# Optimization experiments

Measured on AMD Instinct MI355X. Metric: run time of the kernel, lower is better.

The kernel has to match this reference:

```python
import jax, jax.numpy as jnp
import numpy as np

U, I, D, B, E = 100000, 50000, 64, 4, 2000000

def setup_inputs() -> dict:
    key = jax.random.key(0)
    k1, k2, k3, k4, k5, k6, k7 = jax.random.split(key, 7)
    user_embedding = jax.random.normal(k1, (U, D), dtype=jnp.float32) * 0.1
    item_embedding = jax.random.normal(k2, (I, D), dtype=jnp.float32) * 0.1
    rows = jax.random.randint(k3, (B, E), 0, U, dtype=jnp.int32)
    cols = jax.random.randint(k4, (B, E), 0, I, dtype=jnp.int32)
    # normalized-adjacency-like small positive values
    vals = jax.random.uniform(k5, (B, E), dtype=jnp.float32) * 0.05
    u_w = jax.random.normal(k6, (D, D), dtype=jnp.float32) * (1.0 / np.sqrt(D))
    i_w = jax.random.normal(k7, (D, D), dtype=jnp.float32) * (1.0 / np.sqrt(D))
    return {"user_embedding": user_embedding, "item_embedding": item_embedding,
            "rows": rows, "cols": cols, "vals": vals, "u_w": u_w, "i_w": i_w}

def reference(user_embedding, item_embedding, rows, cols, vals, u_w, i_w):
    n_users = user_embedding.shape[0]
    n_items = item_embedding.shape[0]

    # per-behavior spmm: A @ item_emb -> [U, D]; AT @ user_emb -> [I, D]
    def spmm_user(r, c, v):
        return jax.ops.segment_sum(v[:, None] * item_embedding[c], r,
                                   num_segments=n_users)

    def spmm_item(r, c, v):
        return jax.ops.segment_sum(v[:, None] * user_embedding[r], c,
                                   num_segments=n_items)

    user_stack = jax.vmap(spmm_user)(rows, cols, vals)  # [B, U, D]
    item_stack = jax.vmap(spmm_item)(rows, cols, vals)  # [B, I, D]

    user_emb = jax.nn.sigmoid(jnp.mean(user_stack, axis=0) @ u_w)   # [U, D]
    item_emb = jax.nn.sigmoid(jnp.mean(item_stack, axis=0) @ i_w)   # [I, D]
    user_embs = jax.nn.sigmoid(jnp.einsum('bud,de->bue', user_stack, u_w))  # [B, U, D]
    item_embs = jax.nn.sigmoid(jnp.einsum('bid,de->bie', item_stack, i_w))  # [B, I, D]
    return user_emb, item_emb, user_embs, item_embs
```

## Files before the change

### kernel.cpp

```cpp
#include <hip/hip_runtime.h>

#define U_N 100000
#define I_N 50000
#define D_N 64
#define B_N 4
#define E_N 2000000

#define EDGES   (B_N * E_N)
#define NSC_U   (U_N / 8)
#define NSC_I   (I_N / 8)
#define CROW    12544
#define NBLK    256
#define EPB     (EDGES / NBLK)
#define CAP     1536
#define XSTR    36
#define SC_T    13


__global__ __launch_bounds__(256) void cvt_kernel(const float* __restrict__ ue,
                                                  const float* __restrict__ ie,
                                                  unsigned short* __restrict__ u16,
                                                  unsigned short* __restrict__ i16) {
    int i = blockIdx.x * 256 + threadIdx.x;
    int nu = U_N * D_N;
    int ni = I_N * D_N;
    if (i < nu) {
        unsigned u = __float_as_uint(ue[i]);
        u += 0x7FFFu + ((u >> 16) & 1u);
        u16[i] = (unsigned short)(u >> 16);
    } else if (i < nu + ni) {
        int j = i - nu;
        unsigned u = __float_as_uint(ie[j]);
        u += 0x7FFFu + ((u >> 16) & 1u);
        i16[j] = (unsigned short)(u >> 16);
    }
}

__global__ __launch_bounds__(512) void bhist_kernel(const int* __restrict__ keys,
                                                    int nsc,
                                                    int* __restrict__ cnt) {
    __shared__ int h[CROW];
    for (int i = threadIdx.x; i < nsc; i += 512) h[i] = 0;
    __syncthreads();
    int lb = ((blockIdx.x & 7) << 5) | (blockIdx.x >> 3);
    int base = lb * EPB;
    for (int i = threadIdx.x; i < EPB; i += 512)
        atomicAdd(&h[keys[base + i] >> 3], 1);
    __syncthreads();
    int* row = cnt + (size_t)lb * CROW;
    for (int i = threadIdx.x; i < nsc; i += 512) row[i] = h[i];
}

__global__ __launch_bounds__(512) void scan_tot(const int* __restrict__ cnt,
                                                int nsc, int* __restrict__ cnt_ch) {
    int c = blockIdx.x * 512 + threadIdx.x;
    if (c >= nsc) return;
    int s = 0;
    for (int lb = 0; lb < NBLK; ++lb) s += cnt[(size_t)lb * CROW + c];
    cnt_ch[c] = s;
}

__global__ __launch_bounds__(1024) void scan_ex(const int* __restrict__ cnt_ch,
                                                int nsc, int* __restrict__ off_ch) {
    int t = threadIdx.x;
    int loc[SC_T]; int s = 0;
#pragma unroll
    for (int j = 0; j < SC_T; ++j) {
        int idx = t * SC_T + j;
        int c = (idx < nsc) ? cnt_ch[idx] : 0;
        loc[j] = s; s += c;
    }
    __shared__ int sm[1024];
    int mine = s; sm[t] = s; __syncthreads();
    for (int o = 1; o < 1024; o <<= 1) {
        int a = (t >= o) ? sm[t - o] : 0;
        __syncthreads(); sm[t] += a; __syncthreads();
    }
    int pre = sm[t] - mine;
#pragma unroll
    for (int j = 0; j < SC_T; ++j) {
        int idx = t * SC_T + j;
        if (idx < nsc) off_ch[idx] = pre + loc[j];
    }
}

__global__ __launch_bounds__(512) void scan_cur(int* __restrict__ cnt,
                                                const int* __restrict__ off_ch,
                                                int nsc) {
    int c = blockIdx.x * 512 + threadIdx.x;
    if (c >= nsc) return;
    int run = off_ch[c];
    for (int lb = 0; lb < NBLK; ++lb) {
        int v = cnt[(size_t)lb * CROW + c];
        cnt[(size_t)lb * CROW + c] = run;
        run += v;
    }
}

__global__ __launch_bounds__(512) void cplace_kernel(const int* __restrict__ keys,
                                                     const int* __restrict__ srcs,
                                                     const float* __restrict__ vals,
                                                     const int* __restrict__ cur_g,
                                                     int nsc,
                                                     uint2* __restrict__ pay) {
    __shared__ int cur[CROW];
    int lb = ((blockIdx.x & 7) << 5) | (blockIdx.x >> 3);
    const int* row = cur_g + (size_t)lb * CROW;
    for (int i = threadIdx.x; i < nsc; i += 512) cur[i] = row[i];
    __syncthreads();
    int base = lb * EPB;
    int b = lb >> 6;
    for (int i = threadIdx.x; i < EPB; i += 512) {
        int gi = base + i;
        int k = keys[gi];
        float v = vals[gi];
        int src = srcs[gi];
        int pos = atomicAdd(&cur[k >> 3], 1);
        pay[pos] = make_uint2(((unsigned)(((k & 7) << 2) | b) << 17) | (unsigned)src,
                              __float_as_uint(v));
    }
}

__global__ __launch_bounds__(512) void fused_kernel(
        const unsigned short* __restrict__ emb16,
        const float* __restrict__ W,
        const int* __restrict__ off_ch,
        const int* __restrict__ cnt_ch,
        const uint2* __restrict__ pay,
        float* __restrict__ embs,
        float* __restrict__ mean_out,
        int nrows) {
    int g = blockIdx.x;
    int start = off_ch[g], n = cnt_ch[g];
    int t = threadIdx.x, w = t >> 6, lane = t & 63;

    __shared__ uint2 st[CAP];
    __shared__ uint2 st2[CAP];
    __shared__ int c32[32];
    __shared__ int bstart[33];
    float* xs = (float*)st;

    if (n <= CAP) {
        if (t < 32) c32[t] = 0;
        __syncthreads();
        for (int i = t; i < n; i += 512) {
            uint2 p = pay[start + i];
            st[i] = p;
            atomicAdd(&c32[p.x >> 17], 1);
        }
        __syncthreads();
        if (t == 0) {
            int s = 0;
            for (int b2 = 0; b2 < 32; ++b2) {
                bstart[b2] = s; s += c32[b2]; c32[b2] = bstart[b2];
            }
            bstart[32] = s;
        }
        __syncthreads();
        for (int i = t; i < n; i += 512) {
            uint2 p = st[i];
            int pos = atomicAdd(&c32[p.x >> 17], 1);
            st2[pos] = p;
        }
        __syncthreads();

        int qt = lane >> 4, ql = lane & 15;
        float4 a0, a1, a2, a3;
#define ACC_BIN(AQ, Q)                                                        \
        {                                                                     \
            int s0 = bstart[w * 4 + (Q)], s1 = bstart[w * 4 + (Q) + 1];       \
            AQ = make_float4(0.f, 0.f, 0.f, 0.f);                             \
            for (int j = s0; j < s1; j += 4) {                                \
                int idx = j + qt;                                             \
                int jj = idx < s1 ? idx : s1 - 1;                             \
                uint2 p = st2[jj];                                            \
                float v = (idx < s1) ? __uint_as_float(p.y) : 0.f;            \
                uint2 x = *((const uint2*)(emb16 +                            \
                              (size_t)(p.x & 0x1FFFFu) * 64) + ql);           \
                AQ.x = fmaf(v, __uint_as_float(x.x << 16), AQ.x);             \
                AQ.y = fmaf(v, __uint_as_float(x.x & 0xFFFF0000u), AQ.y);     \
                AQ.z = fmaf(v, __uint_as_float(x.y << 16), AQ.z);             \
                AQ.w = fmaf(v, __uint_as_float(x.y & 0xFFFF0000u), AQ.w);     \
            }                                                                 \
            AQ.x += __shfl_xor(AQ.x, 16); AQ.x += __shfl_xor(AQ.x, 32);       \
            AQ.y += __shfl_xor(AQ.y, 16); AQ.y += __shfl_xor(AQ.y, 32);       \
            AQ.z += __shfl_xor(AQ.z, 16); AQ.z += __shfl_xor(AQ.z, 32);       \
            AQ.w += __shfl_xor(AQ.w, 16); AQ.w += __shfl_xor(AQ.w, 32);       \
        }
        ACC_BIN(a0, 0)
        ACC_BIN(a1, 1)
        ACC_BIN(a2, 2)
        ACC_BIN(a3, 3)
#undef ACC_BIN
        if (qt == 0) {
            *(float4*)&xs[(4 * ql + 0) * XSTR + w * 4] =
                make_float4(a0.x, a1.x, a2.x, a3.x);
            *(float4*)&xs[(4 * ql + 1) * XSTR + w * 4] =
                make_float4(a0.y, a1.y, a2.y, a3.y);
            *(float4*)&xs[(4 * ql + 2) * XSTR + w * 4] =
                make_float4(a0.z, a1.z, a2.z, a3.z);
            *(float4*)&xs[(4 * ql + 3) * XSTR + w * 4] =
                make_float4(a0.w, a1.w, a2.w, a3.w);
        }
    } else {
        for (int i = t; i < 64 * XSTR; i += 512) xs[i] = 0.f;
        __syncthreads();
        for (int j = w; j < n; j += 8) {
            uint2 pv = pay[start + j];
            float x = __uint_as_float(
                (unsigned)emb16[(size_t)(pv.x & 0x1FFFFu) * 64 + lane] << 16);
            atomicAdd(&xs[lane * XSTR + (int)(pv.x >> 17)],
                      __uint_as_float(pv.y) * x);
        }
        __syncthreads();
    }

    float y[4] = {0.f, 0.f, 0.f, 0.f};
#pragma unroll 4
    for (int d = 0; d < 64; ++d) {
        float4 xq = *(const float4*)&xs[d * XSTR + w * 4];
        float wv = W[d * 64 + lane];
        y[0] = fmaf(xq.x, wv, y[0]);
        y[1] = fmaf(xq.y, wv, y[1]);
        y[2] = fmaf(xq.z, wv, y[2]);
        y[3] = fmaf(xq.w, wv, y[3]);
    }
    int row = g * 8 + w;
#pragma unroll
    for (int q = 0; q < 4; ++q)
        embs[((long long)q * nrows + row) * 64 + lane] =
            1.f / (1.f + __expf(-y[q]));
    float m = 0.25f * (y[0] + y[1] + y[2] + y[3]);
    mean_out[(long long)row * 64 + lane] = 1.f / (1.f + __expf(-m));
}

__global__ void scatter_atomic_kernel(const float* __restrict__ user_emb,
                                      const float* __restrict__ item_emb,
                                      const int* __restrict__ rows,
                                      const int* __restrict__ cols,
                                      const float* __restrict__ vals,
                                      float* __restrict__ stack_u,
                                      float* __restrict__ stack_i) {
    long long tid = (long long)blockIdx.x * blockDim.x + threadIdx.x;
    long long e  = tid >> 4;
    int lane = (int)(tid & 15);
    if (e >= (long long)EDGES) return;
    int b = (int)(e / E_N);
    int r = rows[e];
    int c = cols[e];
    float v = vals[e];
    const float4* irow = (const float4*)(item_emb + (long long)c * D_N);
    const float4* urow = (const float4*)(user_emb + (long long)r * D_N);
    float4 iv = irow[lane];
    float4 uv = urow[lane];
    float* du = stack_u + ((long long)b * U_N + r) * D_N + lane * 4;
    float* di = stack_i + ((long long)b * I_N + c) * D_N + lane * 4;
    atomicAdd(du + 0, v * iv.x);
    atomicAdd(du + 1, v * iv.y);
    atomicAdd(du + 2, v * iv.z);
    atomicAdd(du + 3, v * iv.w);
    atomicAdd(di + 0, v * uv.x);
    atomicAdd(di + 1, v * uv.y);
    atomicAdd(di + 2, v * uv.z);
    atomicAdd(di + 3, v * uv.w);
}

template <int NROWS>
__global__ __launch_bounds__(64) void transform_kernel(
        float* __restrict__ stack,
        const float* __restrict__ W,
        float* __restrict__ mean_out) {
    const int row = blockIdx.x;
    const int j   = threadIdx.x;
    __shared__ float xs[B_N][D_N];
#pragma unroll
    for (int b = 0; b < B_N; ++b)
        xs[b][j] = stack[((long long)b * NROWS + row) * D_N + j];
    __syncthreads();
    float acc[B_N] = {0.f, 0.f, 0.f, 0.f};
#pragma unroll 8
    for (int d = 0; d < D_N; ++d) {
        float w = W[d * D_N + j];
#pragma unroll
        for (int b = 0; b < B_N; ++b)
            acc[b] += xs[b][d] * w;
    }
    float m = 0.25f * (acc[0] + acc[1] + acc[2] + acc[3]);
#pragma unroll
    for (int b = 0; b < B_N; ++b)
        stack[((long long)b * NROWS + row) * D_N + j] =
            1.0f / (1.0f + __expf(-acc[b]));
    mean_out[(long long)row * D_N + j] = 1.0f / (1.0f + __expf(-m));
}

extern "C" void kernel_launch(void* const* d_in, const int* in_sizes, int n_in,
                              void* d_out, int out_size, void* d_ws, size_t ws_size,
                              hipStream_t stream) {
    const float* user_emb = (const float*)d_in[0];
    const float* item_emb = (const float*)d_in[1];
    const int*   rows     = (const int*)  d_in[2];
    const int*   cols     = (const int*)  d_in[3];
    const float* vals     = (const float*)d_in[4];
    const float* u_w      = (const float*)d_in[5];
    const float* i_w      = (const float*)d_in[6];

    float* out = (float*)d_out;
    float* user_mean = out;
    float* item_mean = out + (long long)U_N * D_N;
    float* stack_u   = item_mean + (long long)I_N * D_N;
    float* stack_i   = stack_u + (long long)B_N * U_N * D_N;

    int* cnt    = (int*)d_ws;
    int* cnt_ch = cnt + (size_t)NBLK * CROW;
    int* off_ch = cnt_ch + CROW;
    uint2* pay  = (uint2*)(off_ch + CROW);
    unsigned short* user16 = (unsigned short*)(pay + EDGES);
    unsigned short* item16 = user16 + (size_t)U_N * D_N;
    size_t needed = ((size_t)NBLK * CROW + 2 * CROW) * 4 +
                    (size_t)EDGES * 8 + (size_t)(U_N + I_N) * D_N * 2;

    if (ws_size >= needed) {
        int ncvt = (U_N + I_N) * D_N;
        cvt_kernel<<<(ncvt + 255) / 256, 256, 0, stream>>>(user_emb, item_emb,
                                                           user16, item16);
        bhist_kernel<<<NBLK, 512, 0, stream>>>(rows, NSC_U, cnt);
        scan_tot<<<(NSC_U + 511) / 512, 512, 0, stream>>>(cnt, NSC_U, cnt_ch);
        scan_ex<<<1, 1024, 0, stream>>>(cnt_ch, NSC_U, off_ch);
        scan_cur<<<(NSC_U + 511) / 512, 512, 0, stream>>>(cnt, off_ch, NSC_U);
        cplace_kernel<<<NBLK, 512, 0, stream>>>(rows, cols, vals, cnt, NSC_U, pay);
        fused_kernel<<<NSC_U, 512, 0, stream>>>(item16, u_w, off_ch, cnt_ch, pay,
                                                stack_u, user_mean, U_N);
        bhist_kernel<<<NBLK, 512, 0, stream>>>(cols, NSC_I, cnt);
        scan_tot<<<(NSC_I + 511) / 512, 512, 0, stream>>>(cnt, NSC_I, cnt_ch);
        scan_ex<<<1, 1024, 0, stream>>>(cnt_ch, NSC_I, off_ch);
        scan_cur<<<(NSC_I + 511) / 512, 512, 0, stream>>>(cnt, off_ch, NSC_I);
        cplace_kernel<<<NBLK, 512, 0, stream>>>(cols, rows, vals, cnt, NSC_I, pay);
        fused_kernel<<<NSC_I, 512, 0, stream>>>(user16, i_w, off_ch, cnt_ch, pay,
                                                stack_i, item_mean, I_N);
    } else {
        size_t stack_bytes = sizeof(float) * (size_t)B_N * (U_N + I_N) * D_N;
        hipMemsetAsync(stack_u, 0, stack_bytes, stream);
        long long nthreads = (long long)EDGES * 16;
        int nblocks = (int)((nthreads + 255) / 256);
        scatter_atomic_kernel<<<nblocks, 256, 0, stream>>>(
            user_emb, item_emb, rows, cols, vals, stack_u, stack_i);
        transform_kernel<U_N><<<U_N, 64, 0, stream>>>(stack_u, u_w, user_mean);
        transform_kernel<I_N><<<I_N, 64, 0, stream>>>(stack_i, i_w, item_mean);
    }
}
```

Before: 906.7 us.

## Compress sort payload to 4+1 bytes and 16-bit histogram counts

Edge payload shrinks from an 8-byte uint2 to a 4-byte word (bf16 value minus its sign bit, plus a 17-bit source index) and a separate 1-byte local-row/behavior tag. Per-block histograms and cursors are stored as 16-bit values, and the global offset is added inside the placement kernel. The histogram and placement kernels move to 512 blocks of 1024 threads. This is meant to cut global memory traffic in the bucket sort and the gather, at the cost of rounding edge values to bf16 and assuming values are non-negative and per-block counts fit in 16 bits.

```diff
diff --git a/kernel.cpp b/kernel.cpp
--- a/kernel.cpp
+++ b/kernel.cpp
@@ -9,8 +9,8 @@
 #define EDGES   (B_N * E_N)
 #define NSC_U   (U_N / 8)
 #define NSC_I   (I_N / 8)
-#define CROW    12544
-#define NBLK    256
+#define CROW    12500
+#define NBLK    512
 #define EPB     (EDGES / NBLK)
 #define CAP     1536
 #define XSTR    36
@@ -36,27 +36,28 @@
     }
 }
 
-__global__ __launch_bounds__(512) void bhist_kernel(const int* __restrict__ keys,
-                                                    int nsc,
-                                                    int* __restrict__ cnt) {
+__global__ __launch_bounds__(1024) void bhist_kernel(const int* __restrict__ keys,
+                                                     int nsc,
+                                                     unsigned short* __restrict__ cnt16) {
     __shared__ int h[CROW];
-    for (int i = threadIdx.x; i < nsc; i += 512) h[i] = 0;
+    for (int i = threadIdx.x; i < nsc; i += 1024) h[i] = 0;
     __syncthreads();
-    int lb = ((blockIdx.x & 7) << 5) | (blockIdx.x >> 3);
+    int lb = ((blockIdx.x & 7) << 6) | (blockIdx.x >> 3);
     int base = lb * EPB;
-    for (int i = threadIdx.x; i < EPB; i += 512)
+    for (int i = threadIdx.x; i < EPB; i += 1024)
         atomicAdd(&h[keys[base + i] >> 3], 1);
     __syncthreads();
-    int* row = cnt + (size_t)lb * CROW;
-    for (int i = threadIdx.x; i < nsc; i += 512) row[i] = h[i];
-}
-
-__global__ __launch_bounds__(512) void scan_tot(const int* __restrict__ cnt,
-                                                int nsc, int* __restrict__ cnt_ch) {
-    int c = blockIdx.x * 512 + threadIdx.x;
+    unsigned short* row = cnt16 + (size_t)lb * CROW;
+    for (int i = threadIdx.x; i < nsc; i += 1024)
+        row[i] = (unsigned short)h[i];
+}
+
+__global__ __launch_bounds__(1024) void scan_tot(const unsigned short* __restrict__ cnt16,
+                                                 int nsc, int* __restrict__ cnt_ch) {
+    int c = blockIdx.x * 1024 + threadIdx.x;
     if (c >= nsc) return;
     int s = 0;
-    for (int lb = 0; lb < NBLK; ++lb) s += cnt[(size_t)lb * CROW + c];
+    for (int lb = 0; lb < NBLK; ++lb) s += cnt16[(size_t)lb * CROW + c];
     cnt_ch[c] = s;
 }
 
@@ -84,40 +85,44 @@
     }
 }
 
-__global__ __launch_bounds__(512) void scan_cur(int* __restrict__ cnt,
-                                                const int* __restrict__ off_ch,
-                                                int nsc) {
-    int c = blockIdx.x * 512 + threadIdx.x;
+__global__ __launch_bounds__(1024) void scan_cur(const unsigned short* __restrict__ cnt16,
+                                                 unsigned short* __restrict__ cur16,
+                                                 int nsc) {
+    int c = blockIdx.x * 1024 + threadIdx.x;
     if (c >= nsc) return;
-    int run = off_ch[c];
+    int run = 0;
     for (int lb = 0; lb < NBLK; ++lb) {
-        int v = cnt[(size_t)lb * CROW + c];
-        cnt[(size_t)lb * CROW + c] = run;
-        run += v;
-    }
-}
-
-__global__ __launch_bounds__(512) void cplace_kernel(const int* __restrict__ keys,
-                                                     const int* __restrict__ srcs,
-                                                     const float* __restrict__ vals,
-                                                     const int* __restrict__ cur_g,
-                                                     int nsc,
-                                                     uint2* __restrict__ pay) {
+        cur16[(size_t)lb * CROW + c] = (unsigned short)run;
+        run += cnt16[(size_t)lb * CROW + c];
+    }
+}
+
+__global__ __launch_bounds__(1024) void cplace_kernel(const int* __restrict__ keys,
+                                                      const int* __restrict__ srcs,
+                                                      const float* __restrict__ vals,
+                                                      const int* __restrict__ off_ch,
+                                                      const unsigned short* __restrict__ cur16,
+                                                      int nsc,
+                                                      unsigned* __restrict__ payK,
+                                                      unsigned char* __restrict__ payL) {
     __shared__ int cur[CROW];
-    int lb = ((blockIdx.x & 7) << 5) | (blockIdx.x >> 3);
-    const int* row = cur_g + (size_t)lb * CROW;
-    for (int i = threadIdx.x; i < nsc; i += 512) cur[i] = row[i];
+    int lb = ((blockIdx.x & 7) << 6) | (blockIdx.x >> 3);
+    const unsigned short* crow = cur16 + (size_t)lb * CROW;
+    for (int i = threadIdx.x; i < nsc; i += 1024)
+        cur[i] = off_ch[i] + (int)crow[i];
     __syncthreads();
     int base = lb * EPB;
-    int b = lb >> 6;
-    for (int i = threadIdx.x; i < EPB; i += 512) {
+    int b = lb >> 7;
+    for (int i = threadIdx.x; i < EPB; i += 1024) {
         int gi = base + i;
         int k = keys[gi];
-        float v = vals[gi];
+        unsigned u = __float_as_uint(vals[gi]);
+        u += 0x7FFFu + ((u >> 16) & 1u);
+        unsigned bf15 = (u >> 16) & 0x7FFFu;
         int src = srcs[gi];
         int pos = atomicAdd(&cur[k >> 3], 1);
-        pay[pos] = make_uint2(((unsigned)(((k & 7) << 2) | b) << 17) | (unsigned)src,
-                              __float_as_uint(v));
+        payK[pos] = (bf15 << 17) | (unsigned)src;
+        payL[pos] = (unsigned char)(((k & 7) << 2) | b);
     }
 }
 
@@ -126,7 +131,8 @@
         const float* __restrict__ W,
         const int* __restrict__ off_ch,
         const int* __restrict__ cnt_ch,
-        const uint2* __restrict__ pay,
+        const unsigned* __restrict__ payK,
+        const unsigned char* __restrict__ payL,
         float* __restrict__ embs,
         float* __restrict__ mean_out,
         int nrows) {
@@ -134,20 +140,16 @@
     int start = off_ch[g], n = cnt_ch[g];
     int t = threadIdx.x, w = t >> 6, lane = t & 63;
 
-    __shared__ uint2 st[CAP];
-    __shared__ uint2 st2[CAP];
+    __shared__ unsigned st2[CAP];
+    __shared__ float xs[64 * XSTR];
     __shared__ int c32[32];
     __shared__ int bstart[33];
-    float* xs = (float*)st;
 
     if (n <= CAP) {
         if (t < 32) c32[t] = 0;
         __syncthreads();
-        for (int i = t; i < n; i += 512) {
-            uint2 p = pay[start + i];
-            st[i] = p;
-            atomicAdd(&c32[p.x >> 17], 1);
-        }
+        for (int i = t; i < n; i += 512)
+            atomicAdd(&c32[payL[start + i]], 1);
         __syncthreads();
         if (t == 0) {
             int s = 0;
@@ -158,9 +160,8 @@
         }
         __syncthreads();
         for (int i = t; i < n; i += 512) {
-            uint2 p = st[i];
-            int pos = atomicAdd(&c32[p.x >> 17], 1);
-            st2[pos] = p;
+            int pos = atomicAdd(&c32[payL[start + i]], 1);
+            st2[pos] = payK[start + i];
         }
         __syncthreads();
 
@@ -173,10 +174,11 @@
             for (int j = s0; j < s1; j += 4) {                                \
                 int idx = j + qt;                                             \
                 int jj = idx < s1 ? idx : s1 - 1;                             \
-                uint2 p = st2[jj];                                            \
-                float v = (idx < s1) ? __uint_as_float(p.y) : 0.f;            \
+                unsigned p = st2[jj];                                         \
+                float v = (idx < s1)                                          \
+                    ? __uint_as_float((p & 0xFFFE0000u) >> 1) : 0.f;          \
                 uint2 x = *((const uint2*)(emb16 +                            \
-                              (size_t)(p.x & 0x1FFFFu) * 64) + ql);           \
+                              (size_t)(p & 0x1FFFFu) * 64) + ql);             \
                 AQ.x = fmaf(v, __uint_as_float(x.x << 16), AQ.x);             \
                 AQ.y = fmaf(v, __uint_as_float(x.x & 0xFFFF0000u), AQ.y);     \
                 AQ.z = fmaf(v, __uint_as_float(x.y << 16), AQ.z);             \
@@ -206,11 +208,12 @@
         for (int i = t; i < 64 * XSTR; i += 512) xs[i] = 0.f;
         __syncthreads();
         for (int j = w; j < n; j += 8) {
-            uint2 pv = pay[start + j];
+            unsigned p = payK[start + j];
+            int local = payL[start + j];
+            float v = __uint_as_float((p & 0xFFFE0000u) >> 1);
             float x = __uint_as_float(
-                (unsigned)emb16[(size_t)(pv.x & 0x1FFFFu) * 64 + lane] << 16);
-            atomicAdd(&xs[lane * XSTR + (int)(pv.x >> 17)],
-                      __uint_as_float(pv.y) * x);
+                (unsigned)emb16[(size_t)(p & 0x1FFFFu) * 64 + lane] << 16);
+            atomicAdd(&xs[lane * XSTR + local], v * x);
         }
         __syncthreads();
     }
@@ -310,33 +313,37 @@
     float* stack_u   = item_mean + (long long)I_N * D_N;
     float* stack_i   = stack_u + (long long)B_N * U_N * D_N;
 
-    int* cnt    = (int*)d_ws;
-    int* cnt_ch = cnt + (size_t)NBLK * CROW;
+    unsigned* payK = (unsigned*)d_ws;
+    unsigned short* user16 = (unsigned short*)(payK + EDGES);
+    unsigned short* item16 = user16 + (size_t)U_N * D_N;
+    unsigned short* cnt16  = item16 + (size_t)I_N * D_N;
+    unsigned short* cur16  = cnt16 + (size_t)NBLK * CROW;
+    unsigned char*  payL   = (unsigned char*)(cur16 + (size_t)NBLK * CROW);
+    int* cnt_ch = (int*)(payL + (size_t)EDGES);
     int* off_ch = cnt_ch + CROW;
-    uint2* pay  = (uint2*)(off_ch + CROW);
-    unsigned short* user16 = (unsigned short*)(pay + EDGES);
-    unsigned short* item16 = user16 + (size_t)U_N * D_N;
-    size_t needed = ((size_t)NBLK * CROW + 2 * CROW) * 4 +
-                    (size_t)EDGES * 8 + (size_t)(U_N + I_N) * D_N * 2;
+    size_t needed = (size_t)EDGES * 4 + (size_t)(U_N + I_N) * D_N * 2 +
+                    (size_t)NBLK * CROW * 4 + (size_t)EDGES + CROW * 8;
 
     if (ws_size >= needed) {
         int ncvt = (U_N + I_N) * D_N;
         cvt_kernel<<<(ncvt + 255) / 256, 256, 0, stream>>>(user_emb, item_emb,
                                                            user16, item16);
-        bhist_kernel<<<NBLK, 512, 0, stream>>>(rows, NSC_U, cnt);
-        scan_tot<<<(NSC_U + 511) / 512, 512, 0, stream>>>(cnt, NSC_U, cnt_ch);
+        bhist_kernel<<<NBLK, 1024, 0, stream>>>(rows, NSC_U, cnt16);
+        scan_tot<<<(NSC_U + 1023) / 1024, 1024, 0, stream>>>(cnt16, NSC_U, cnt_ch);
         scan_ex<<<1, 1024, 0, stream>>>(cnt_ch, NSC_U, off_ch);
-        scan_cur<<<(NSC_U + 511) / 512, 512, 0, stream>>>(cnt, off_ch, NSC_U);
-        cplace_kernel<<<NBLK, 512, 0, stream>>>(rows, cols, vals, cnt, NSC_U, pay);
-        fused_kernel<<<NSC_U, 512, 0, stream>>>(item16, u_w, off_ch, cnt_ch, pay,
-                                                stack_u, user_mean, U_N);
-        bhist_kernel<<<NBLK, 512, 0, stream>>>(cols, NSC_I, cnt);
-        scan_tot<<<(NSC_I + 511) / 512, 512, 0, stream>>>(cnt, NSC_I, cnt_ch);
+        scan_cur<<<(NSC_U + 1023) / 1024, 1024, 0, stream>>>(cnt16, cur16, NSC_U);
+        cplace_kernel<<<NBLK, 1024, 0, stream>>>(rows, cols, vals, off_ch, cur16,
+                                                 NSC_U, payK, payL);
+        fused_kernel<<<NSC_U, 512, 0, stream>>>(item16, u_w, off_ch, cnt_ch,
+                                                payK, payL, stack_u, user_mean, U_N);
+        bhist_kernel<<<NBLK, 1024, 0, stream>>>(cols, NSC_I, cnt16);
+        scan_tot<<<(NSC_I + 1023) / 1024, 1024, 0, stream>>>(cnt16, NSC_I, cnt_ch);
         scan_ex<<<1, 1024, 0, stream>>>(cnt_ch, NSC_I, off_ch);
-        scan_cur<<<(NSC_I + 511) / 512, 512, 0, stream>>>(cnt, off_ch, NSC_I);
-        cplace_kernel<<<NBLK, 512, 0, stream>>>(cols, rows, vals, cnt, NSC_I, pay);
-        fused_kernel<<<NSC_I, 512, 0, stream>>>(user16, i_w, off_ch, cnt_ch, pay,
-                                                stack_i, item_mean, I_N);
+        scan_cur<<<(NSC_I + 1023) / 1024, 1024, 0, stream>>>(cnt16, cur16, NSC_I);
+        cplace_kernel<<<NBLK, 1024, 0, stream>>>(cols, rows, vals, off_ch, cur16,
+                                                 NSC_I, payK, payL);
+        fused_kernel<<<NSC_I, 512, 0, stream>>>(user16, i_w, off_ch, cnt_ch,
+                                                payK, payL, stack_i, item_mean, I_N);
     } else {
         size_t stack_bytes = sizeof(float) * (size_t)B_N * (U_N + I_N) * D_N;
         hipMemsetAsync(stack_u, 0, stack_bytes, stream);
```

After: 1.095 ms. +20.7%, slower.

## Premultiply embeddings by weight matrices before SpMM to drop per-row GEMV

Applied to the files above, without the earlier changes.

Uses linearity (A·X)·W = A·(X·W) to precompute X·W for item and user embeddings in a new kernel that also rounds to bf16. The fused SpMM kernel then applies sigmoid directly to the accumulated sums and writes vectorised outputs, removing the 64x64 transform loop and the staging shared buffer. Payload entries are read twice from global memory instead of being cached in LDS. This trades the per-output GEMV for a GEMV per input row. Rounding X·W rather than X to bf16 changes the numerical error profile.

```diff
diff --git a/kernel.cpp b/kernel.cpp
--- a/kernel.cpp
+++ b/kernel.cpp
@@ -13,26 +13,30 @@
 #define NBLK    256
 #define EPB     (EDGES / NBLK)
 #define CAP     1536
-#define XSTR    36
 #define SC_T    13
 
 
-__global__ __launch_bounds__(256) void cvt_kernel(const float* __restrict__ ue,
-                                                  const float* __restrict__ ie,
-                                                  unsigned short* __restrict__ u16,
-                                                  unsigned short* __restrict__ i16) {
-    int i = blockIdx.x * 256 + threadIdx.x;
-    int nu = U_N * D_N;
-    int ni = I_N * D_N;
-    if (i < nu) {
-        unsigned u = __float_as_uint(ue[i]);
-        u += 0x7FFFu + ((u >> 16) & 1u);
-        u16[i] = (unsigned short)(u >> 16);
-    } else if (i < nu + ni) {
-        int j = i - nu;
-        unsigned u = __float_as_uint(ie[j]);
-        u += 0x7FFFu + ((u >> 16) & 1u);
-        i16[j] = (unsigned short)(u >> 16);
+__global__ __launch_bounds__(256) void precompW_kernel(
+        const float* __restrict__ emb, const float* __restrict__ W,
+        unsigned short* __restrict__ out16, int nrows) {
+    __shared__ float Wl[4096];
+    int t = threadIdx.x, w = t >> 6, lane = t & 63;
+    for (int i = t; i < 4096; i += 256) Wl[i] = W[i];
+    __syncthreads();
+    int base = blockIdx.x * 32;
+#pragma unroll
+    for (int it = 0; it < 8; ++it) {
+        int row = base + it * 4 + w;
+        float x = (row < nrows) ? emb[row * 64 + lane] : 0.f;
+        float y = 0.f;
+#pragma unroll 8
+        for (int d = 0; d < 64; ++d)
+            y = fmaf(__shfl(x, d), Wl[d * 64 + lane], y);
+        if (row < nrows) {
+            unsigned u = __float_as_uint(y);
+            u += 0x7FFFu + ((u >> 16) & 1u);
+            out16[row * 64 + lane] = (unsigned short)(u >> 16);
+        }
     }
 }
 
@@ -122,8 +126,7 @@
 }
 
 __global__ __launch_bounds__(512) void fused_kernel(
-        const unsigned short* __restrict__ emb16,
-        const float* __restrict__ W,
+        const unsigned short* __restrict__ embW16,
         const int* __restrict__ off_ch,
         const int* __restrict__ cnt_ch,
         const uint2* __restrict__ pay,
@@ -134,20 +137,16 @@
     int start = off_ch[g], n = cnt_ch[g];
     int t = threadIdx.x, w = t >> 6, lane = t & 63;
 
-    __shared__ uint2 st[CAP];
     __shared__ uint2 st2[CAP];
     __shared__ int c32[32];
     __shared__ int bstart[33];
-    float* xs = (float*)st;
+    float* ys = (float*)st2;
 
     if (n <= CAP) {
         if (t < 32) c32[t] = 0;
         __syncthreads();
-        for (int i = t; i < n; i += 512) {
-            uint2 p = pay[start + i];
-            st[i] = p;
-            atomicAdd(&c32[p.x >> 17], 1);
-        }
+        for (int i = t; i < n; i += 512)
+            atomicAdd(&c32[pay[start + i].x >> 17], 1);
         __syncthreads();
         if (t == 0) {
             int s = 0;
@@ -158,7 +157,7 @@
         }
         __syncthreads();
         for (int i = t; i < n; i += 512) {
-            uint2 p = st[i];
+            uint2 p = pay[start + i];
             int pos = atomicAdd(&c32[p.x >> 17], 1);
             st2[pos] = p;
         }
@@ -175,7 +174,7 @@
                 int jj = idx < s1 ? idx : s1 - 1;                             \
                 uint2 p = st2[jj];                                            \
                 float v = (idx < s1) ? __uint_as_float(p.y) : 0.f;            \
-                uint2 x = *((const uint2*)(emb16 +                            \
+                uint2 x = *((const uint2*)(embW16 +                           \
                               (size_t)(p.x & 0x1FFFFu) * 64) + ql);           \
                 AQ.x = fmaf(v, __uint_as_float(x.x << 16), AQ.x);             \
                 AQ.y = fmaf(v, __uint_as_float(x.x & 0xFFFF0000u), AQ.y);     \
@@ -193,45 +192,50 @@
         ACC_BIN(a3, 3)
 #undef ACC_BIN
         if (qt == 0) {
-            *(float4*)&xs[(4 * ql + 0) * XSTR + w * 4] =
-                make_float4(a0.x, a1.x, a2.x, a3.x);
-            *(float4*)&xs[(4 * ql + 1) * XSTR + w * 4] =
-                make_float4(a0.y, a1.y, a2.y, a3.y);
-            *(float4*)&xs[(4 * ql + 2) * XSTR + w * 4] =
-                make_float4(a0.z, a1.z, a2.z, a3.z);
-            *(float4*)&xs[(4 * ql + 3) * XSTR + w * 4] =
-                make_float4(a0.w, a1.w, a2.w, a3.w);
+            int row = g * 8 + w;
+            float4 yq[4] = {a0, a1, a2, a3};
+#pragma unroll
+            for (int q = 0; q < 4; ++q) {
+                float4 s4;
+                s4.x = 1.f / (1.f + __expf(-yq[q].x));
+                s4.y = 1.f / (1.f + __expf(-yq[q].y));
+                s4.z = 1.f / (1.f + __expf(-yq[q].z));
+                s4.w = 1.f / (1.f + __expf(-yq[q].w));
+                *(float4*)&embs[((long long)q * nrows + row) * 64 + 4 * ql] = s4;
+            }
+            float4 m4;
+            m4.x = 0.25f * (a0.x + a1.x + a2.x + a3.x);
+            m4.y = 0.25f * (a0.y + a1.y + a2.y + a3.y);
+            m4.z = 0.25f * (a0.z + a1.z + a2.z + a3.z);
+            m4.w = 0.25f * (a0.w + a1.w + a2.w + a3.w);
+            m4.x = 1.f / (1.f + __expf(-m4.x));
+            m4.y = 1.f / (1.f + __expf(-m4.y));
+            m4.z = 1.f / (1.f + __expf(-m4.z));
+            m4.w = 1.f / (1.f + __expf(-m4.w));
+            *(float4*)&mean_out[(long long)row * 64 + 4 * ql] = m4;
         }
     } else {
-        for (int i = t; i < 64 * XSTR; i += 512) xs[i] = 0.f;
+        for (int i = t; i < 2048; i += 512) ys[i] = 0.f;
         __syncthreads();
         for (int j = w; j < n; j += 8) {
             uint2 pv = pay[start + j];
             float x = __uint_as_float(
-                (unsigned)emb16[(size_t)(pv.x & 0x1FFFFu) * 64 + lane] << 16);
-            atomicAdd(&xs[lane * XSTR + (int)(pv.x >> 17)],
+                (unsigned)embW16[(size_t)(pv.x & 0x1FFFFu) * 64 + lane] << 16);
+            atomicAdd(&ys[(pv.x >> 17) * 64 + lane],
                       __uint_as_float(pv.y) * x);
         }
         __syncthreads();
-    }
-
-    float y[4] = {0.f, 0.f, 0.f, 0.f};
-#pragma unroll 4
-    for (int d = 0; d < 64; ++d) {
-        float4 xq = *(const float4*)&xs[d * XSTR + w * 4];
-        float wv = W[d * 64 + lane];
-        y[0] = fmaf(xq.x, wv, y[0]);
-        y[1] = fmaf(xq.y, wv, y[1]);
-        y[2] = fmaf(xq.z, wv, y[2]);
-        y[3] = fmaf(xq.w, wv, y[3]);
-    }
-    int row = g * 8 + w;
-#pragma unroll
-    for (int q = 0; q < 4; ++q)
-        embs[((long long)q * nrows + row) * 64 + lane] =
-            1.f / (1.f + __expf(-y[q]));
-    float m = 0.25f * (y[0] + y[1] + y[2] + y[3]);
-    mean_out[(long long)row * 64 + lane] = 1.f / (1.f + __expf(-m));
+        int row = g * 8 + w;
+        float y[4];
+#pragma unroll
+        for (int q = 0; q < 4; ++q) {
+            y[q] = ys[(w * 4 + q) * 64 + lane];
+            embs[((long long)q * nrows + row) * 64 + lane] =
+                1.f / (1.f + __expf(-y[q]));
+        }
+        float m = 0.25f * (y[0] + y[1] + y[2] + y[3]);
+        mean_out[(long long)row * 64 + lane] = 1.f / (1.f + __expf(-m));
+    }
 }
 
 __global__ void scatter_atomic_kernel(const float* __restrict__ user_emb,
@@ -314,28 +318,29 @@
     int* cnt_ch = cnt + (size_t)NBLK * CROW;
     int* off_ch = cnt_ch + CROW;
     uint2* pay  = (uint2*)(off_ch + CROW);
-    unsigned short* user16 = (unsigned short*)(pay + EDGES);
-    unsigned short* item16 = user16 + (size_t)U_N * D_N;
+    unsigned short* userW16 = (unsigned short*)(pay + EDGES);
+    unsigned short* itemW16 = userW16 + (size_t)U_N * D_N;
     size_t needed = ((size_t)NBLK * CROW + 2 * CROW) * 4 +
                     (size_t)EDGES * 8 + (size_t)(U_N + I_N) * D_N * 2;
 
     if (ws_size >= needed) {
-        int ncvt = (U_N + I_N) * D_N;
-        cvt_kernel<<<(ncvt + 255) / 256, 256, 0, stream>>>(user_emb, item_emb,
-                                                           user16, item16);
+        precompW_kernel<<<(I_N + 31) / 32, 256, 0, stream>>>(item_emb, u_w,
+                                                             itemW16, I_N);
+        precompW_kernel<<<(U_N + 31) / 32, 256, 0, stream>>>(user_emb, i_w,
+                                                             userW16, U_N);
         bhist_kernel<<<NBLK, 512, 0, stream>>>(rows, NSC_U, cnt);
         scan_tot<<<(NSC_U + 511) / 512, 512, 0, stream>>>(cnt, NSC_U, cnt_ch);
         scan_ex<<<1, 1024, 0, stream>>>(cnt_ch, NSC_U, off_ch);
         scan_cur<<<(NSC_U + 511) / 512, 512, 0, stream>>>(cnt, off_ch, NSC_U);
         cplace_kernel<<<NBLK, 512, 0, stream>>>(rows, cols, vals, cnt, NSC_U, pay);
-        fused_kernel<<<NSC_U, 512, 0, stream>>>(item16, u_w, off_ch, cnt_ch, pay,
+        fused_kernel<<<NSC_U, 512, 0, stream>>>(itemW16, off_ch, cnt_ch, pay,
                                                 stack_u, user_mean, U_N);
         bhist_kernel<<<NBLK, 512, 0, stream>>>(cols, NSC_I, cnt);
         scan_tot<<<(NSC_I + 511) / 512, 512, 0, stream>>>(cnt, NSC_I, cnt_ch);
         scan_ex<<<1, 1024, 0, stream>>>(cnt_ch, NSC_I, off_ch);
         scan_cur<<<(NSC_I + 511) / 512, 512, 0, stream>>>(cnt, off_ch, NSC_I);
         cplace_kernel<<<NBLK, 512, 0, stream>>>(cols, rows, vals, cnt, NSC_I, pay);
-        fused_kernel<<<NSC_I, 512, 0, stream>>>(user16, i_w, off_ch, cnt_ch, pay,
+        fused_kernel<<<NSC_I, 512, 0, stream>>>(userW16, off_ch, cnt_ch, pay,
                                                 stack_i, item_mean, I_N);
     } else {
         size_t stack_bytes = sizeof(float) * (size_t)B_N * (U_N + I_N) * D_N;
```

Measured after the change: 996.3 us. +9.9%, slower.
